# Kernel tuning notes

Hardware: AMD Instinct MI355X
Metric: run time of the kernel (lower is better)

## Reference

```python
import jax, jax.numpy as jnp
import numpy as np

B, NB, T, C, H, FW, TW = 4, 64, 512, 256, 8, 8, 8
HD = C // H
SCALE = HD ** -0.5
EPS = 1e-5


def setup_inputs() -> dict:
    key = jax.random.key(0)
    ks = jax.random.split(key, 12)
    inpt = jax.random.normal(ks[0], (B, NB, T, C), jnp.float32)
    perm_n = jax.vmap(lambda k: jax.random.permutation(k, NB))(jax.random.split(ks[1], B)).astype(jnp.int32)
    perm_t = jax.vmap(lambda k: jax.random.permutation(k, T))(jax.random.split(ks[2], B)).astype(jnp.int32)
    w = lambda k, shp: (jax.random.normal(k, shp, jnp.float32) * 0.02)
    return {
        "inpt": inpt, "perm_n": perm_n, "perm_t": perm_t,
        "ln_g": jnp.ones((C,), jnp.float32), "ln_b": jnp.zeros((C,), jnp.float32),
        "Wq": w(ks[3], (C, C)), "bq": jnp.zeros((C,), jnp.float32),
        "Wk": w(ks[4], (C, C)), "bk": jnp.zeros((C,), jnp.float32),
        "Wv": w(ks[5], (C, C)), "bv": jnp.zeros((C,), jnp.float32),
        "Wp": w(ks[6], (C, C)), "bp": jnp.zeros((C,), jnp.float32),
    }


def _layernorm(x, g, b):
    m = x.mean(-1, keepdims=True)
    v = ((x - m) ** 2).mean(-1, keepdims=True)
    return (x - m) * jax.lax.rsqrt(v + EPS) * g + b


def reference(inpt, perm_n, perm_t, ln_g, ln_b, Wq, bq, Wk, bk, Wv, bv, Wp, bp):
    x = _layernorm(inpt, ln_g, ln_b)  # (B, NB, T, C)

    # per-batch shuffle: gather along N then along T
    shuffled = jax.vmap(lambda xb, pn, pt: xb[pn][:, pt])(x, perm_n, perm_t)

    # window partition -> (B*NB/FW*T/TW, FW*TW, C)
    win = shuffled.reshape(B, NB // FW, FW, T // TW, TW, C)
    win = win.transpose(0, 1, 3, 2, 4, 5).reshape(-1, FW * TW, C)

    def heads(y):  # (Bw, L, C) -> (Bw, H, L, HD)
        return y.reshape(y.shape[0], y.shape[1], H, HD).transpose(0, 2, 1, 3)

    q = heads(win @ Wq.T + bq) * SCALE
    k = heads(win @ Wk.T + bk)
    v = heads(win @ Wv.T + bv)

    attn = jax.nn.softmax(jnp.einsum('bhqd,bhkd->bhqk', q, k), axis=-1)
    o = jnp.einsum('bhqk,bhkd->bhqd', attn, v)
    o = o.transpose(0, 2, 1, 3).reshape(-1, FW * TW, C)
    o = o @ Wp.T + bp

    # window reverse -> (B, NB, T, C)
    y = o.reshape(B, NB // FW, T // TW, FW, TW, C)
    y = y.transpose(0, 1, 3, 2, 4, 5).reshape(B, NB, T, C)

    # scatter reverse == gather with inverse permutations
    inv_n = jnp.argsort(perm_n, axis=-1)
    inv_t = jnp.argsort(perm_t, axis=-1)
    unshuf = jax.vmap(lambda yb, qn, qt: yb[:, qt][qn])(y, inv_n, inv_t)

    return inpt + unshuf
```

## Files before the change

kernel.cpp:

```cpp
#include <hip/hip_runtime.h>

typedef __attribute__((ext_vector_type(4))) float f32x4;
typedef __attribute__((ext_vector_type(8))) short bf16x8;

#define EPS_ 1e-5f
#define QSC 0.25503639409729144f

#define LDS_BYTES 32768

__device__ __forceinline__ int swzx(int r, int c) { return r * 256 + (c ^ ((r & 7) << 3)); }

__device__ __forceinline__ unsigned int pack2(float a, float b) {
  union { float f; unsigned int u; } ua, ub;
  ua.f = a; ub.f = b;
  unsigned int ra = (ua.u + 0x7FFFu + ((ua.u >> 16) & 1u)) >> 16;
  unsigned int rb = (ub.u + 0x7FFFu + ((ub.u >> 16) & 1u)) & 0xFFFF0000u;
  return ra | rb;
}
__device__ __forceinline__ uint2 pack4(f32x4 v) {
  uint2 o; o.x = pack2(v[0], v[1]); o.y = pack2(v[2], v[3]); return o;
}
__device__ __forceinline__ unsigned short f2b(float f) {
  union { float f; unsigned int u; } c; c.f = f;
  return (unsigned short)((c.u + 0x7FFFu + ((c.u >> 16) & 1u)) >> 16);
}

__device__ __forceinline__ bf16x8 xform(f32x4 A0, f32x4 A1, int ae, int ao, bool hi) {
  int P0 = (int)pack2(A0[0], A0[1]), P1 = (int)pack2(A0[2], A0[3]);
  int P2 = (int)pack2(A1[0], A1[1]), P3 = (int)pack2(A1[2], A1[3]);
  int e0 = __builtin_amdgcn_ds_bpermute(ae, P0);
  int e1 = __builtin_amdgcn_ds_bpermute(ae, P1);
  int e2 = __builtin_amdgcn_ds_bpermute(ae, P2);
  int e3 = __builtin_amdgcn_ds_bpermute(ae, P3);
  int o0 = __builtin_amdgcn_ds_bpermute(ao, P0);
  int o1 = __builtin_amdgcn_ds_bpermute(ao, P1);
  int o2 = __builtin_amdgcn_ds_bpermute(ao, P2);
  int o3 = __builtin_amdgcn_ds_bpermute(ao, P3);
  union { bf16x8 v; int u[4]; } r;
  r.u[0] = hi ? e2 : e0;
  r.u[1] = hi ? e3 : e1;
  r.u[2] = hi ? o2 : o0;
  r.u[3] = hi ? o3 : o1;
  return r.v;
}

__global__ __launch_bounds__(256) void k0_cvt(const float* __restrict__ w0,
                                              const float* __restrict__ w1,
                                              const float* __restrict__ w2,
                                              const float* __restrict__ w3,
                                              unsigned short* __restrict__ dst) {
  int idx = blockIdx.x * 256 + threadIdx.x;
  const float* s = (blockIdx.y == 0) ? w0 : (blockIdx.y == 1) ? w1 : (blockIdx.y == 2) ? w2 : w3;
  dst[blockIdx.y * 65536 + idx] = f2b(s[idx]);
}

__global__ __launch_bounds__(256, 3) void ka_fused(
    const unsigned short* __restrict__ Wall,
    const float* __restrict__ ln_g, const float* __restrict__ ln_b,
    const int* __restrict__ pn, const int* __restrict__ pt,
    const float* __restrict__ bq, const float* __restrict__ bk,
    const float* __restrict__ bv, const float* __restrict__ bp,
    const float* __restrict__ inpt, float* __restrict__ out) {
  extern __shared__ unsigned short lds[];

  const int tid = threadIdx.x;
  const int wv = tid >> 6, lane = tid & 63, quad = lane >> 4, l15 = lane & 15;
  const int w = blockIdx.x;
  const int b = w >> 9, nbb = (w >> 6) & 7, tbb = w & 63;
  const f32x4 z4 = {0.f, 0.f, 0.f, 0.f};

  const int ae = ((((quad << 1) & 3) << 4) + l15) << 2;
  const int ao = (((((quad << 1) + 1) & 3) << 4) + l15) << 2;
  const bool hi = lane >= 32;

  {
    const float4 gg = ((const float4*)ln_g)[lane];
    const float4 bb = ((const float4*)ln_b)[lane];
    #pragma unroll
    for (int ii = 0; ii < 2; ++ii) {
      const int nloc = wv * 2 + ii;
      const int spn = pn[(b << 6) + (nbb << 3) + nloc];
      const float* rowbase = inpt + (size_t)((b << 6) + spn) * 512 * 256;
      float4 v[8];
      #pragma unroll
      for (int i = 0; i < 8; ++i) {
        const int spt = pt[(b << 9) + (tbb << 3) + i];
        v[i] = ((const float4*)(rowbase + (size_t)spt * 256))[lane];
      }
      #pragma unroll
      for (int i = 0; i < 8; ++i) {
        float s = v[i].x + v[i].y + v[i].z + v[i].w;
        float ss = v[i].x * v[i].x + v[i].y * v[i].y + v[i].z * v[i].z + v[i].w * v[i].w;
        #pragma unroll
        for (int m = 1; m < 64; m <<= 1) { s += __shfl_xor(s, m); ss += __shfl_xor(ss, m); }
        const float mean = s * (1.0f / 256.0f);
        const float rs = rsqrtf(ss * (1.0f / 256.0f) - mean * mean + EPS_);
        ushort4 o;
        o.x = f2b((v[i].x - mean) * rs * gg.x + bb.x);
        o.y = f2b((v[i].y - mean) * rs * gg.y + bb.y);
        o.z = f2b((v[i].z - mean) * rs * gg.z + bb.z);
        o.w = f2b((v[i].w - mean) * rs * gg.w + bb.w);
        const int row = nloc * 8 + i;
        *(ushort4*)(lds + swzx(row, lane * 4)) = o;
      }
    }
  }
  __syncthreads();

  const unsigned short* Wq = Wall;
  const unsigned short* Wk = Wall + 65536;
  const unsigned short* Wv_ = Wall + 131072;
  const unsigned short* Wp = Wall + 196608;

  uint2 opk[2][2][4];

  #pragma unroll
  for (int hh = 0; hh < 2; ++hh) {
    const int h = (wv << 1) + hh;

    bf16x8 kf[4], vf[2][2];
    {
      f32x4 ka_[2][4], va[4][2];
      #pragma unroll
      for (int m2 = 0; m2 < 2; ++m2)
        #pragma unroll
        for (int nt = 0; nt < 4; ++nt) { ka_[m2][nt] = z4; va[nt][m2] = z4; }

      __builtin_amdgcn_s_setprio(1);
      #pragma unroll
      for (int ks = 0; ks < 8; ++ks) {
        bf16x8 bx[4];
        #pragma unroll
        for (int nt = 0; nt < 4; ++nt)
          bx[nt] = *(const bf16x8*)(lds + swzx(nt * 16 + l15, ks * 32 + quad * 8));
        #pragma unroll
        for (int m2 = 0; m2 < 2; ++m2) {
          const int wrow = (h * 32 + m2 * 16 + l15) * 256 + ks * 32 + quad * 8;
          bf16x8 wk8 = *(const bf16x8*)(Wk + wrow);
          bf16x8 wv8 = *(const bf16x8*)(Wv_ + wrow);
          #pragma unroll
          for (int nt = 0; nt < 4; ++nt) {
            ka_[m2][nt] = __builtin_amdgcn_mfma_f32_16x16x32_bf16(wk8, bx[nt], ka_[m2][nt], 0, 0, 0);
            va[nt][m2] = __builtin_amdgcn_mfma_f32_16x16x32_bf16(bx[nt], wv8, va[nt][m2], 0, 0, 0);
          }
        }
      }
      __builtin_amdgcn_s_setprio(0);

      #pragma unroll
      for (int m2 = 0; m2 < 2; ++m2) {
        const float4 bk4 = ((const float4*)(bk + h * 32 + m2 * 16))[quad];
        const float bvv = bv[h * 32 + m2 * 16 + l15];
        #pragma unroll
        for (int nt = 0; nt < 4; ++nt) {
          ka_[m2][nt][0] += bk4.x; ka_[m2][nt][1] += bk4.y;
          ka_[m2][nt][2] += bk4.z; ka_[m2][nt][3] += bk4.w;
          va[nt][m2][0] += bvv; va[nt][m2][1] += bvv;
          va[nt][m2][2] += bvv; va[nt][m2][3] += bvv;
        }
      }
      #pragma unroll
      for (int i = 0; i < 4; ++i) kf[i] = xform(ka_[0][i], ka_[1][i], ae, ao, hi);
      #pragma unroll
      for (int kk = 0; kk < 2; ++kk)
        #pragma unroll
        for (int m2 = 0; m2 < 2; ++m2)
          vf[kk][m2] = xform(va[2 * kk][m2], va[2 * kk + 1][m2], ae, ao, hi);
    }

    bf16x8 qf[4];
    {
      f32x4 qa[2][4];
      #pragma unroll
      for (int m2 = 0; m2 < 2; ++m2)
        #pragma unroll
        for (int nt = 0; nt < 4; ++nt) qa[m2][nt] = z4;

      __builtin_amdgcn_s_setprio(1);
      #pragma unroll
      for (int ks = 0; ks < 8; ++ks) {
        bf16x8 bx[4];
        #pragma unroll
        for (int nt = 0; nt < 4; ++nt)
          bx[nt] = *(const bf16x8*)(lds + swzx(nt * 16 + l15, ks * 32 + quad * 8));
        #pragma unroll
        for (int m2 = 0; m2 < 2; ++m2) {
          const int wrow = (h * 32 + m2 * 16 + l15) * 256 + ks * 32 + quad * 8;
          bf16x8 wq8 = *(const bf16x8*)(Wq + wrow);
          #pragma unroll
          for (int nt = 0; nt < 4; ++nt)
            qa[m2][nt] = __builtin_amdgcn_mfma_f32_16x16x32_bf16(wq8, bx[nt], qa[m2][nt], 0, 0, 0);
        }
      }
      __builtin_amdgcn_s_setprio(0);

      #pragma unroll
      for (int m2 = 0; m2 < 2; ++m2) {
        const float4 bq4 = ((const float4*)(bq + h * 32 + m2 * 16))[quad];
        #pragma unroll
        for (int nt = 0; nt < 4; ++nt) {
          qa[m2][nt][0] = (qa[m2][nt][0] + bq4.x) * QSC;
          qa[m2][nt][1] = (qa[m2][nt][1] + bq4.y) * QSC;
          qa[m2][nt][2] = (qa[m2][nt][2] + bq4.z) * QSC;
          qa[m2][nt][3] = (qa[m2][nt][3] + bq4.w) * QSC;
        }
      }
      #pragma unroll
      for (int i = 0; i < 4; ++i) qf[i] = xform(qa[0][i], qa[1][i], ae, ao, hi);
    }

    float tot[4] = {0.f, 0.f, 0.f, 0.f};
    bf16x8 pb[2][4];
    #pragma unroll
    for (int kk = 0; kk < 2; ++kk)
      #pragma unroll
      for (int ntq = 0; ntq < 4; ++ntq) {
        f32x4 s0 = __builtin_amdgcn_mfma_f32_16x16x32_bf16(kf[2 * kk], qf[ntq], z4, 0, 0, 0);
        f32x4 s1 = __builtin_amdgcn_mfma_f32_16x16x32_bf16(kf[2 * kk + 1], qf[ntq], z4, 0, 0, 0);
        #pragma unroll
        for (int r = 0; r < 4; ++r) {
          s0[r] = __builtin_amdgcn_exp2f(s0[r]); tot[ntq] += s0[r];
          s1[r] = __builtin_amdgcn_exp2f(s1[r]); tot[ntq] += s1[r];
        }
        pb[kk][ntq] = xform(s0, s1, ae, ao, hi);
      }
    float inv[4];
    #pragma unroll
    for (int ntq = 0; ntq < 4; ++ntq) {
      float t = tot[ntq];
      t += __shfl_xor(t, 16);
      t += __shfl_xor(t, 32);
      inv[ntq] = 1.0f / t;
    }

    __builtin_amdgcn_s_setprio(1);
    #pragma unroll
    for (int m2 = 0; m2 < 2; ++m2)
      #pragma unroll
      for (int ntq = 0; ntq < 4; ++ntq) {
        f32x4 oa = __builtin_amdgcn_mfma_f32_16x16x32_bf16(vf[0][m2], pb[0][ntq], z4, 0, 0, 0);
        oa = __builtin_amdgcn_mfma_f32_16x16x32_bf16(vf[1][m2], pb[1][ntq], oa, 0, 0, 0);
        oa[0] *= inv[ntq]; oa[1] *= inv[ntq]; oa[2] *= inv[ntq]; oa[3] *= inv[ntq];
        opk[hh][m2][ntq] = pack4(oa);
      }
    __builtin_amdgcn_s_setprio(0);
  }

  __syncthreads();
  #pragma unroll
  for (int hh = 0; hh < 2; ++hh)
    #pragma unroll
    for (int m2 = 0; m2 < 2; ++m2)
      #pragma unroll
      for (int ntq = 0; ntq < 4; ++ntq)
        *(uint2*)(lds + swzx(ntq * 16 + l15, ((wv * 2 + hh) * 32 + m2 * 16 + quad * 4))) =
            opk[hh][m2][ntq];
  __syncthreads();

  f32x4 pacc[4][4];
  #pragma unroll
  for (int m4 = 0; m4 < 4; ++m4)
    #pragma unroll
    for (int nto = 0; nto < 4; ++nto) pacc[m4][nto] = z4;
  __builtin_amdgcn_s_setprio(1);
  #pragma unroll
  for (int ks = 0; ks < 8; ++ks) {
    bf16x8 ob[4];
    #pragma unroll
    for (int nto = 0; nto < 4; ++nto)
      ob[nto] = *(const bf16x8*)(lds + swzx(nto * 16 + l15, ks * 32 + quad * 8));
    #pragma unroll
    for (int m4 = 0; m4 < 4; ++m4) {
      bf16x8 wp8 = *(const bf16x8*)(Wp + (wv * 64 + m4 * 16 + l15) * 256 + ks * 32 + quad * 8);
      #pragma unroll
      for (int nto = 0; nto < 4; ++nto)
        pacc[m4][nto] = __builtin_amdgcn_mfma_f32_16x16x32_bf16(wp8, ob[nto], pacc[m4][nto], 0, 0, 0);
    }
  }
  __builtin_amdgcn_s_setprio(0);

  int toff[4];
  #pragma unroll
  for (int nto = 0; nto < 4; ++nto) {
    const int tok = nto * 16 + l15;
    const int n = (nbb << 3) + (tok >> 3), t = (tbb << 3) + (tok & 7);
    toff[nto] = (((b << 6) + pn[(b << 6) + n]) * 512 + pt[(b << 9) + t]) * 256;
  }
  #pragma unroll
  for (int m4 = 0; m4 < 4; ++m4) {
    float4 bp4 = ((const float4*)(bp + wv * 64 + m4 * 16))[quad];
    #pragma unroll
    for (int nto = 0; nto < 4; ++nto) {
      const int off = toff[nto] + wv * 64 + m4 * 16 + quad * 4;
      float4 iv = *(const float4*)(inpt + off);
      float4 o;
      o.x = iv.x + pacc[m4][nto][0] + bp4.x;
      o.y = iv.y + pacc[m4][nto][1] + bp4.y;
      o.z = iv.z + pacc[m4][nto][2] + bp4.z;
      o.w = iv.w + pacc[m4][nto][3] + bp4.w;
      *(float4*)(out + off) = o;
    }
  }
}

extern "C" void kernel_launch(void* const* d_in, const int* in_sizes, int n_in,
                              void* d_out, int out_size, void* d_ws, size_t ws_size,
                              hipStream_t stream) {
  const float* inpt = (const float*)d_in[0];
  const int* perm_n = (const int*)d_in[1];
  const int* perm_t = (const int*)d_in[2];
  const float* ln_g = (const float*)d_in[3];
  const float* ln_b = (const float*)d_in[4];
  const float* Wq = (const float*)d_in[5];
  const float* bq = (const float*)d_in[6];
  const float* Wk = (const float*)d_in[7];
  const float* bk = (const float*)d_in[8];
  const float* Wv = (const float*)d_in[9];
  const float* bv = (const float*)d_in[10];
  const float* Wp = (const float*)d_in[11];
  const float* bp = (const float*)d_in[12];
  float* out = (float*)d_out;

  unsigned short* Wall = (unsigned short*)d_ws;

  (void)hipFuncSetAttribute((const void*)ka_fused,
                            hipFuncAttributeMaxDynamicSharedMemorySize, LDS_BYTES);

  k0_cvt<<<dim3(256, 4), 256, 0, stream>>>(Wq, Wk, Wv, Wp, Wall);
  ka_fused<<<2048, 256, LDS_BYTES, stream>>>(Wall, ln_g, ln_b, perm_n, perm_t,
                                             bq, bk, bv, bp, inpt, out);
}
```

Measured before the change: 410.0 us.

## Use 512-thread blocks with one head per wave

The fused window-attention kernel now launches 8 waves per block instead of 4. Each wave handles one attention head, one N row of the layernorm load, and 32 output channels of the projection, where before each wave looped over two heads. This aims to raise parallelism and latency hiding by lowering per-wave register pressure and serial work. The cost is more waves competing for the same LDS and more block-wide barrier participants. The launch bounds change from (256,3) to (512,4), which caps registers per thread more tightly.

Result: faster. 399.3 us (-2.6%).

```diff
diff --git a/kernel.cpp b/kernel.cpp
--- a/kernel.cpp
+++ b/kernel.cpp
@@ -54,7 +54,7 @@
   dst[blockIdx.y * 65536 + idx] = f2b(s[idx]);
 }
 
-__global__ __launch_bounds__(256, 3) void ka_fused(
+__global__ __launch_bounds__(512, 4) void ka_fused(
     const unsigned short* __restrict__ Wall,
     const float* __restrict__ ln_g, const float* __restrict__ ln_b,
     const int* __restrict__ pn, const int* __restrict__ pt,
@@ -76,33 +76,28 @@
   {
     const float4 gg = ((const float4*)ln_g)[lane];
     const float4 bb = ((const float4*)ln_b)[lane];
-    #pragma unroll
-    for (int ii = 0; ii < 2; ++ii) {
-      const int nloc = wv * 2 + ii;
-      const int spn = pn[(b << 6) + (nbb << 3) + nloc];
-      const float* rowbase = inpt + (size_t)((b << 6) + spn) * 512 * 256;
-      float4 v[8];
-      #pragma unroll
-      for (int i = 0; i < 8; ++i) {
-        const int spt = pt[(b << 9) + (tbb << 3) + i];
-        v[i] = ((const float4*)(rowbase + (size_t)spt * 256))[lane];
-      }
-      #pragma unroll
-      for (int i = 0; i < 8; ++i) {
-        float s = v[i].x + v[i].y + v[i].z + v[i].w;
-        float ss = v[i].x * v[i].x + v[i].y * v[i].y + v[i].z * v[i].z + v[i].w * v[i].w;
-        #pragma unroll
-        for (int m = 1; m < 64; m <<= 1) { s += __shfl_xor(s, m); ss += __shfl_xor(ss, m); }
-        const float mean = s * (1.0f / 256.0f);
-        const float rs = rsqrtf(ss * (1.0f / 256.0f) - mean * mean + EPS_);
-        ushort4 o;
-        o.x = f2b((v[i].x - mean) * rs * gg.x + bb.x);
-        o.y = f2b((v[i].y - mean) * rs * gg.y + bb.y);
-        o.z = f2b((v[i].z - mean) * rs * gg.z + bb.z);
-        o.w = f2b((v[i].w - mean) * rs * gg.w + bb.w);
-        const int row = nloc * 8 + i;
-        *(ushort4*)(lds + swzx(row, lane * 4)) = o;
-      }
+    const int spn = pn[(b << 6) + (nbb << 3) + wv];
+    const float* rowbase = inpt + (size_t)((b << 6) + spn) * 512 * 256;
+    float4 v[8];
+    #pragma unroll
+    for (int i = 0; i < 8; ++i) {
+      const int spt = pt[(b << 9) + (tbb << 3) + i];
+      v[i] = ((const float4*)(rowbase + (size_t)spt * 256))[lane];
+    }
+    #pragma unroll
+    for (int i = 0; i < 8; ++i) {
+      float s = v[i].x + v[i].y + v[i].z + v[i].w;
+      float ss = v[i].x * v[i].x + v[i].y * v[i].y + v[i].z * v[i].z + v[i].w * v[i].w;
+      #pragma unroll
+      for (int m = 1; m < 64; m <<= 1) { s += __shfl_xor(s, m); ss += __shfl_xor(ss, m); }
+      const float mean = s * (1.0f / 256.0f);
+      const float rs = rsqrtf(ss * (1.0f / 256.0f) - mean * mean + EPS_);
+      ushort4 o;
+      o.x = f2b((v[i].x - mean) * rs * gg.x + bb.x);
+      o.y = f2b((v[i].y - mean) * rs * gg.y + bb.y);
+      o.z = f2b((v[i].z - mean) * rs * gg.z + bb.z);
+      o.w = f2b((v[i].w - mean) * rs * gg.w + bb.w);
+      *(ushort4*)(lds + swzx(wv * 8 + i, lane * 4)) = o;
     }
   }
   __syncthreads();
@@ -111,157 +106,149 @@
   const unsigned short* Wk = Wall + 65536;
   const unsigned short* Wv_ = Wall + 131072;
   const unsigned short* Wp = Wall + 196608;
-
-  uint2 opk[2][2][4];
-
-  #pragma unroll
-  for (int hh = 0; hh < 2; ++hh) {
-    const int h = (wv << 1) + hh;
-
-    bf16x8 kf[4], vf[2][2];
-    {
-      f32x4 ka_[2][4], va[4][2];
+  const int h = wv;
+
+  bf16x8 kf[4], vf[2][2];
+  {
+    f32x4 ka_[2][4], va[4][2];
+    #pragma unroll
+    for (int m2 = 0; m2 < 2; ++m2)
+      #pragma unroll
+      for (int nt = 0; nt < 4; ++nt) { ka_[m2][nt] = z4; va[nt][m2] = z4; }
+
+    __builtin_amdgcn_s_setprio(1);
+    #pragma unroll
+    for (int ks = 0; ks < 8; ++ks) {
+      bf16x8 bx[4];
+      #pragma unroll
+      for (int nt = 0; nt < 4; ++nt)
+        bx[nt] = *(const bf16x8*)(lds + swzx(nt * 16 + l15, ks * 32 + quad * 8));
+      #pragma unroll
+      for (int m2 = 0; m2 < 2; ++m2) {
+        const int wrow = (h * 32 + m2 * 16 + l15) * 256 + ks * 32 + quad * 8;
+        bf16x8 wk8 = *(const bf16x8*)(Wk + wrow);
+        bf16x8 wv8 = *(const bf16x8*)(Wv_ + wrow);
+        #pragma unroll
+        for (int nt = 0; nt < 4; ++nt) {
+          ka_[m2][nt] = __builtin_amdgcn_mfma_f32_16x16x32_bf16(wk8, bx[nt], ka_[m2][nt], 0, 0, 0);
+          va[nt][m2] = __builtin_amdgcn_mfma_f32_16x16x32_bf16(bx[nt], wv8, va[nt][m2], 0, 0, 0);
+        }
+      }
+    }
+    __builtin_amdgcn_s_setprio(0);
+
+    #pragma unroll
+    for (int m2 = 0; m2 < 2; ++m2) {
+      const float4 bk4 = ((const float4*)(bk + h * 32 + m2 * 16))[quad];
+      const float bvv = bv[h * 32 + m2 * 16 + l15];
+      #pragma unroll
+      for (int nt = 0; nt < 4; ++nt) {
+        ka_[m2][nt][0] += bk4.x; ka_[m2][nt][1] += bk4.y;
+        ka_[m2][nt][2] += bk4.z; ka_[m2][nt][3] += bk4.w;
+        va[nt][m2][0] += bvv; va[nt][m2][1] += bvv;
+        va[nt][m2][2] += bvv; va[nt][m2][3] += bvv;
+      }
+    }
+    #pragma unroll
+    for (int i = 0; i < 4; ++i) kf[i] = xform(ka_[0][i], ka_[1][i], ae, ao, hi);
+    #pragma unroll
+    for (int kk = 0; kk < 2; ++kk)
       #pragma unroll
       for (int m2 = 0; m2 < 2; ++m2)
-        #pragma unroll
-        for (int nt = 0; nt < 4; ++nt) { ka_[m2][nt] = z4; va[nt][m2] = z4; }
-
-      __builtin_amdgcn_s_setprio(1);
-      #pragma unroll
-      for (int ks = 0; ks < 8; ++ks) {
-        bf16x8 bx[4];
+        vf[kk][m2] = xform(va[2 * kk][m2], va[2 * kk + 1][m2], ae, ao, hi);
+  }
+
+  bf16x8 qf[4];
+  {
+    f32x4 qa[2][4];
+    #pragma unroll
+    for (int m2 = 0; m2 < 2; ++m2)
+      #pragma unroll
+      for (int nt = 0; nt < 4; ++nt) qa[m2][nt] = z4;
+
+    __builtin_amdgcn_s_setprio(1);
+    #pragma unroll
+    for (int ks = 0; ks < 8; ++ks) {
+      bf16x8 bx[4];
+      #pragma unroll
+      for (int nt = 0; nt < 4; ++nt)
+        bx[nt] = *(const bf16x8*)(lds + swzx(nt * 16 + l15, ks * 32 + quad * 8));
+      #pragma unroll
+      for (int m2 = 0; m2 < 2; ++m2) {
+        const int wrow = (h * 32 + m2 * 16 + l15) * 256 + ks * 32 + quad * 8;
+        bf16x8 wq8 = *(const bf16x8*)(Wq + wrow);
         #pragma unroll
         for (int nt = 0; nt < 4; ++nt)
-          bx[nt] = *(const bf16x8*)(lds + swzx(nt * 16 + l15, ks * 32 + quad * 8));
-        #pragma unroll
-        for (int m2 = 0; m2 < 2; ++m2) {
-          const int wrow = (h * 32 + m2 * 16 + l15) * 256 + ks * 32 + quad * 8;
-          bf16x8 wk8 = *(const bf16x8*)(Wk + wrow);
-          bf16x8 wv8 = *(const bf16x8*)(Wv_ + wrow);
-          #pragma unroll
-          for (int nt = 0; nt < 4; ++nt) {
-            ka_[m2][nt] = __builtin_amdgcn_mfma_f32_16x16x32_bf16(wk8, bx[nt], ka_[m2][nt], 0, 0, 0);
-            va[nt][m2] = __builtin_amdgcn_mfma_f32_16x16x32_bf16(bx[nt], wv8, va[nt][m2], 0, 0, 0);
-          }
-        }
-      }
-      __builtin_amdgcn_s_setprio(0);
-
-      #pragma unroll
-      for (int m2 = 0; m2 < 2; ++m2) {
-        const float4 bk4 = ((const float4*)(bk + h * 32 + m2 * 16))[quad];
-        const float bvv = bv[h * 32 + m2 * 16 + l15];
-        #pragma unroll
-        for (int nt = 0; nt < 4; ++nt) {
-          ka_[m2][nt][0] += bk4.x; ka_[m2][nt][1] += bk4.y;
-          ka_[m2][nt][2] += bk4.z; ka_[m2][nt][3] += bk4.w;
-          va[nt][m2][0] += bvv; va[nt][m2][1] += bvv;
-          va[nt][m2][2] += bvv; va[nt][m2][3] += bvv;
-        }
-      }
-      #pragma unroll
-      for (int i = 0; i < 4; ++i) kf[i] = xform(ka_[0][i], ka_[1][i], ae, ao, hi);
-      #pragma unroll
-      for (int kk = 0; kk < 2; ++kk)
-        #pragma unroll
-        for (int m2 = 0; m2 < 2; ++m2)
-          vf[kk][m2] = xform(va[2 * kk][m2], va[2 * kk + 1][m2], ae, ao, hi);
-    }
-
-    bf16x8 qf[4];
-    {
-      f32x4 qa[2][4];
-      #pragma unroll
-      for (int m2 = 0; m2 < 2; ++m2)
-        #pragma unroll
-        for (int nt = 0; nt < 4; ++nt) qa[m2][nt] = z4;
-
-      __builtin_amdgcn_s_setprio(1);
-      #pragma unroll
-      for (int ks = 0; ks < 8; ++ks) {
-        bf16x8 bx[4];
-        #pragma unroll
-        for (int nt = 0; nt < 4; ++nt)
-          bx[nt] = *(const bf16x8*)(lds + swzx(nt * 16 + l15, ks * 32 + quad * 8));
-        #pragma unroll
-        for (int m2 = 0; m2 < 2; ++m2) {
-          const int wrow = (h * 32 + m2 * 16 + l15) * 256 + ks * 32 + quad * 8;
-          bf16x8 wq8 = *(const bf16x8*)(Wq + wrow);
-          #pragma unroll
-          for (int nt = 0; nt < 4; ++nt)
-            qa[m2][nt] = __builtin_amdgcn_mfma_f32_16x16x32_bf16(wq8, bx[nt], qa[m2][nt], 0, 0, 0);
-        }
-      }
-      __builtin_amdgcn_s_setprio(0);
-
-      #pragma unroll
-      for (int m2 = 0; m2 < 2; ++m2) {
-        const float4 bq4 = ((const float4*)(bq + h * 32 + m2 * 16))[quad];
-        #pragma unroll
-        for (int nt = 0; nt < 4; ++nt) {
-          qa[m2][nt][0] = (qa[m2][nt][0] + bq4.x) * QSC;
-          qa[m2][nt][1] = (qa[m2][nt][1] + bq4.y) * QSC;
-          qa[m2][nt][2] = (qa[m2][nt][2] + bq4.z) * QSC;
-          qa[m2][nt][3] = (qa[m2][nt][3] + bq4.w) * QSC;
-        }
-      }
-      #pragma unroll
-      for (int i = 0; i < 4; ++i) qf[i] = xform(qa[0][i], qa[1][i], ae, ao, hi);
-    }
-
-    float tot[4] = {0.f, 0.f, 0.f, 0.f};
-    bf16x8 pb[2][4];
-    #pragma unroll
-    for (int kk = 0; kk < 2; ++kk)
-      #pragma unroll
-      for (int ntq = 0; ntq < 4; ++ntq) {
-        f32x4 s0 = __builtin_amdgcn_mfma_f32_16x16x32_bf16(kf[2 * kk], qf[ntq], z4, 0, 0, 0);
-        f32x4 s1 = __builtin_amdgcn_mfma_f32_16x16x32_bf16(kf[2 * kk + 1], qf[ntq], z4, 0, 0, 0);
-        #pragma unroll
-        for (int r = 0; r < 4; ++r) {
-          s0[r] = __builtin_amdgcn_exp2f(s0[r]); tot[ntq] += s0[r];
-          s1[r] = __builtin_amdgcn_exp2f(s1[r]); tot[ntq] += s1[r];
-        }
-        pb[kk][ntq] = xform(s0, s1, ae, ao, hi);
-      }
-    float inv[4];
+          qa[m2][nt] = __builtin_amdgcn_mfma_f32_16x16x32_bf16(wq8, bx[nt], qa[m2][nt], 0, 0, 0);
+      }
+    }
+    __builtin_amdgcn_s_setprio(0);
+
+    #pragma unroll
+    for (int m2 = 0; m2 < 2; ++m2) {
+      const float4 bq4 = ((const float4*)(bq + h * 32 + m2 * 16))[quad];
+      #pragma unroll
+      for (int nt = 0; nt < 4; ++nt) {
+        qa[m2][nt][0] = (qa[m2][nt][0] + bq4.x) * QSC;
+        qa[m2][nt][1] = (qa[m2][nt][1] + bq4.y) * QSC;
+        qa[m2][nt][2] = (qa[m2][nt][2] + bq4.z) * QSC;
+        qa[m2][nt][3] = (qa[m2][nt][3] + bq4.w) * QSC;
+      }
+    }
+    #pragma unroll
+    for (int i = 0; i < 4; ++i) qf[i] = xform(qa[0][i], qa[1][i], ae, ao, hi);
+  }
+
+  float tot[4] = {0.f, 0.f, 0.f, 0.f};
+  bf16x8 pb[2][4];
+  #pragma unroll
+  for (int kk = 0; kk < 2; ++kk)
     #pragma unroll
     for (int ntq = 0; ntq < 4; ++ntq) {
-      float t = tot[ntq];
-      t += __shfl_xor(t, 16);
-      t += __shfl_xor(t, 32);
-      inv[ntq] = 1.0f / t;
-    }
-
-    __builtin_amdgcn_s_setprio(1);
-    #pragma unroll
-    for (int m2 = 0; m2 < 2; ++m2)
-      #pragma unroll
-      for (int ntq = 0; ntq < 4; ++ntq) {
-        f32x4 oa = __builtin_amdgcn_mfma_f32_16x16x32_bf16(vf[0][m2], pb[0][ntq], z4, 0, 0, 0);
-        oa = __builtin_amdgcn_mfma_f32_16x16x32_bf16(vf[1][m2], pb[1][ntq], oa, 0, 0, 0);
-        oa[0] *= inv[ntq]; oa[1] *= inv[ntq]; oa[2] *= inv[ntq]; oa[3] *= inv[ntq];
-        opk[hh][m2][ntq] = pack4(oa);
-      }
-    __builtin_amdgcn_s_setprio(0);
-  }
+      f32x4 s0 = __builtin_amdgcn_mfma_f32_16x16x32_bf16(kf[2 * kk], qf[ntq], z4, 0, 0, 0);
+      f32x4 s1 = __builtin_amdgcn_mfma_f32_16x16x32_bf16(kf[2 * kk + 1], qf[ntq], z4, 0, 0, 0);
+      #pragma unroll
+      for (int r = 0; r < 4; ++r) {
+        s0[r] = __builtin_amdgcn_exp2f(s0[r]); tot[ntq] += s0[r];
+        s1[r] = __builtin_amdgcn_exp2f(s1[r]); tot[ntq] += s1[r];
+      }
+      pb[kk][ntq] = xform(s0, s1, ae, ao, hi);
+    }
+  float inv[4];
+  #pragma unroll
+  for (int ntq = 0; ntq < 4; ++ntq) {
+    float t = tot[ntq];
+    t += __shfl_xor(t, 16);
+    t += __shfl_xor(t, 32);
+    inv[ntq] = 1.0f / t;
+  }
+
+  uint2 opk[2][4];
+  __builtin_amdgcn_s_setprio(1);
+  #pragma unroll
+  for (int m2 = 0; m2 < 2; ++m2)
+    #pragma unroll
+    for (int ntq = 0; ntq < 4; ++ntq) {
+      f32x4 oa = __builtin_amdgcn_mfma_f32_16x16x32_bf16(vf[0][m2], pb[0][ntq], z4, 0, 0, 0);
+      oa = __builtin_amdgcn_mfma_f32_16x16x32_bf16(vf[1][m2], pb[1][ntq], oa, 0, 0, 0);
+      oa[0] *= inv[ntq]; oa[1] *= inv[ntq]; oa[2] *= inv[ntq]; oa[3] *= inv[ntq];
+      opk[m2][ntq] = pack4(oa);
+    }
+  __builtin_amdgcn_s_setprio(0);
 
   __syncthreads();
   #pragma unroll
-  for (int hh = 0; hh < 2; ++hh)
-    #pragma unroll
-    for (int m2 = 0; m2 < 2; ++m2)
-      #pragma unroll
-      for (int ntq = 0; ntq < 4; ++ntq)
-        *(uint2*)(lds + swzx(ntq * 16 + l15, ((wv * 2 + hh) * 32 + m2 * 16 + quad * 4))) =
-            opk[hh][m2][ntq];
+  for (int m2 = 0; m2 < 2; ++m2)
+    #pragma unroll
+    for (int ntq = 0; ntq < 4; ++ntq)
+      *(uint2*)(lds + swzx(ntq * 16 + l15, (h * 32 + m2 * 16 + quad * 4))) = opk[m2][ntq];
   __syncthreads();
 
-  f32x4 pacc[4][4];
-  #pragma unroll
-  for (int m4 = 0; m4 < 4; ++m4)
-    #pragma unroll
-    for (int nto = 0; nto < 4; ++nto) pacc[m4][nto] = z4;
+  f32x4 pacc[2][4];
+  #pragma unroll
+  for (int m2 = 0; m2 < 2; ++m2)
+    #pragma unroll
+    for (int nto = 0; nto < 4; ++nto) pacc[m2][nto] = z4;
   __builtin_amdgcn_s_setprio(1);
   #pragma unroll
   for (int ks = 0; ks < 8; ++ks) {
@@ -270,11 +257,11 @@
     for (int nto = 0; nto < 4; ++nto)
       ob[nto] = *(const bf16x8*)(lds + swzx(nto * 16 + l15, ks * 32 + quad * 8));
     #pragma unroll
-    for (int m4 = 0; m4 < 4; ++m4) {
-      bf16x8 wp8 = *(const bf16x8*)(Wp + (wv * 64 + m4 * 16 + l15) * 256 + ks * 32 + quad * 8);
+    for (int m2 = 0; m2 < 2; ++m2) {
+      bf16x8 wp8 = *(const bf16x8*)(Wp + (wv * 32 + m2 * 16 + l15) * 256 + ks * 32 + quad * 8);
       #pragma unroll
       for (int nto = 0; nto < 4; ++nto)
-        pacc[m4][nto] = __builtin_amdgcn_mfma_f32_16x16x32_bf16(wp8, ob[nto], pacc[m4][nto], 0, 0, 0);
+        pacc[m2][nto] = __builtin_amdgcn_mfma_f32_16x16x32_bf16(wp8, ob[nto], pacc[m2][nto], 0, 0, 0);
     }
   }
   __builtin_amdgcn_s_setprio(0);
@@ -287,17 +274,17 @@
     toff[nto] = (((b << 6) + pn[(b << 6) + n]) * 512 + pt[(b << 9) + t]) * 256;
   }
   #pragma unroll
-  for (int m4 = 0; m4 < 4; ++m4) {
-    float4 bp4 = ((const float4*)(bp + wv * 64 + m4 * 16))[quad];
+  for (int m2 = 0; m2 < 2; ++m2) {
+    float4 bp4 = ((const float4*)(bp + wv * 32 + m2 * 16))[quad];
     #pragma unroll
     for (int nto = 0; nto < 4; ++nto) {
-      const int off = toff[nto] + wv * 64 + m4 * 16 + quad * 4;
+      const int off = toff[nto] + wv * 32 + m2 * 16 + quad * 4;
       float4 iv = *(const float4*)(inpt + off);
       float4 o;
-      o.x = iv.x + pacc[m4][nto][0] + bp4.x;
-      o.y = iv.y + pacc[m4][nto][1] + bp4.y;
-      o.z = iv.z + pacc[m4][nto][2] + bp4.z;
-      o.w = iv.w + pacc[m4][nto][3] + bp4.w;
+      o.x = iv.x + pacc[m2][nto][0] + bp4.x;
+      o.y = iv.y + pacc[m2][nto][1] + bp4.y;
+      o.z = iv.z + pacc[m2][nto][2] + bp4.z;
+      o.w = iv.w + pacc[m2][nto][3] + bp4.w;
       *(float4*)(out + off) = o;
     }
   }
@@ -327,6 +314,6 @@
                             hipFuncAttributeMaxDynamicSharedMemorySize, LDS_BYTES);
 
   k0_cvt<<<dim3(256, 4), 256, 0, stream>>>(Wq, Wk, Wv, Wp, Wall);
-  ka_fused<<<2048, 256, LDS_BYTES, stream>>>(Wall, ln_g, ln_b, perm_n, perm_t,
+  ka_fused<<<2048, 512, LDS_BYTES, stream>>>(Wall, ln_g, ln_b, perm_n, perm_t,
                                              bq, bk, bv, bp, inpt, out);
 }
```
